# Optimization experiments

Hardware: AMD Instinct MI355X
Metric: run time of the kernel (lower is better)

The kernel has to match this reference:

```python
import jax, jax.numpy as jnp
import numpy as np

N_NODES = 50000
N_EDGES = 800000
N_GRAPHS = 256
IN_DIM = 128
HID = 128
BN_EPS = 1e-5


def setup_inputs() -> dict:
    key = jax.random.key(0)
    ks = jax.random.split(key, 12)
    s = 1.0 / np.sqrt(HID)
    feats = jax.random.normal(ks[0], (N_NODES, IN_DIM), jnp.float32)
    src = jax.random.randint(ks[1], (2, N_EDGES), 0, N_NODES)
    dst = jax.random.randint(ks[2], (2, N_EDGES), 0, N_NODES)
    graph_ids = jnp.sort(jax.random.randint(ks[3], (N_NODES,), 0, N_GRAPHS))
    eps = jnp.full((2, 2), 0.1, jnp.float32)
    Wa = jax.random.normal(ks[4], (2, 2, IN_DIM, HID), jnp.float32) * s
    ba = jnp.zeros((2, 2, HID), jnp.float32)
    bng = jnp.ones((2, 2, HID), jnp.float32)
    bnb = jnp.zeros((2, 2, HID), jnp.float32)
    Wb = jax.random.normal(ks[5], (2, 2, HID, HID), jnp.float32) * s
    bb = jnp.zeros((2, 2, HID), jnp.float32)
    oW1 = jax.random.normal(ks[6], (2 * HID, HID), jnp.float32) * (1.0 / np.sqrt(2 * HID))
    ob1 = jnp.zeros((HID,), jnp.float32)
    oW2 = jax.random.normal(ks[7], (HID, HID), jnp.float32) * s
    ob2 = jnp.zeros((HID,), jnp.float32)
    oW3 = jax.random.normal(ks[8], (HID, 1), jnp.float32) * s
    ob3 = jnp.zeros((1,), jnp.float32)
    return {"feats": feats, "src": src, "dst": dst, "graph_ids": graph_ids,
            "n_graphs": N_GRAPHS, "eps": eps, "Wa": Wa, "ba": ba, "bng": bng,
            "bnb": bnb, "Wb": Wb, "bb": bb, "oW1": oW1, "ob1": ob1,
            "oW2": oW2, "ob2": ob2, "oW3": oW3, "ob3": ob3}


def _gin_layer(h, s, d, eps_l, Wa_l, ba_l, g_l, be_l, Wb_l, bb_l, relu_out):
    # sum-aggregate messages from src to dst over edge list
    N = h.shape[0]
    agg = jax.ops.segment_sum(h[s], d, num_segments=N)  # [N, D]
    x = (1.0 + eps_l) * h + agg
    # MLP_Layer: Linear -> BatchNorm(training stats) -> ReLU -> Linear
    x = x @ Wa_l + ba_l
    mu = jnp.mean(x, axis=0)
    var = jnp.var(x, axis=0)
    x = (x - mu) * jax.lax.rsqrt(var + BN_EPS) * g_l + be_l
    x = jax.nn.relu(x)
    x = x @ Wb_l + bb_l
    return jax.nn.relu(x) if relu_out else x  # GINConv activation (gin1 only)


def reference(feats, src, dst, graph_ids, n_graphs, eps, Wa, ba, bng, bnb,
              Wb, bb, oW1, ob1, oW2, ob2, oW3, ob3):
    outs = []
    for e in range(2):  # one BTGINs encoder per bottom edge type
        h = feats
        for l in range(2):  # gin1 (ReLU) then gin2 (no activation)
            h = _gin_layer(h, src[e], dst[e], eps[e, l], Wa[e, l], ba[e, l],
                           bng[e, l], bnb[e, l], Wb[e, l], bb[e, l], relu_out=(l == 0))
        outs.append(h)
    h = jnp.concatenate(outs, axis=-1)  # [N, 2*HID]
    # readout_nodes op='sum': per-graph segment sum
    hg = jax.ops.segment_sum(h, graph_ids, num_segments=n_graphs)  # [G, 2*HID]
    # out_layers: 3-layer MLP, no BN
    x = jax.nn.relu(hg @ oW1 + ob1)
    x = jax.nn.relu(x @ oW2 + ob2)
    return x @ oW3 + ob3  # [G, 1]
```

## Files before the change

kernel.cpp:

```cpp
#include <hip/hip_runtime.h>

#define NT 50000
#define NE 800000
#define NG 256
#define DIM 128
#define GEMM_B ((NT + 127) / 128)

#define NB 128
#define BW 391
#define PB 196
#define PCH 4096
#define HCN (NB * PB)

typedef short s16x8 __attribute__((ext_vector_type(8)));
typedef float f32x16 __attribute__((ext_vector_type(16)));

__device__ __forceinline__ unsigned short f32_to_bf16(float f) {
    unsigned int u = __float_as_uint(f);
    u += 0x7FFFu + ((u >> 16) & 1u);
    return (unsigned short)(u >> 16);
}
__device__ __forceinline__ float bf16_to_f32(unsigned short h) {
    return __uint_as_float(((unsigned int)h) << 16);
}

__global__ __launch_bounds__(256) void tobf16_kernel(const float* __restrict__ in,
                                                     unsigned short* __restrict__ out) {
    int i = blockIdx.x * 256 + threadIdx.x;
    if (i >= NT * 32) return;
    float4 v = ((const float4*)in)[i];
    ushort4 o;
    o.x = f32_to_bf16(v.x); o.y = f32_to_bf16(v.y);
    o.z = f32_to_bf16(v.z); o.w = f32_to_bf16(v.w);
    ((ushort4*)out)[i] = o;
}

__global__ __launch_bounds__(256) void csr_part_hist_kernel(
        const int* __restrict__ dstAll, int* __restrict__ hcoarseAll) {
    const int* dst = dstAll + (size_t)blockIdx.y * NE;
    int* hcoarse = hcoarseAll + (size_t)blockIdx.y * HCN;
    __shared__ int h[NB];
    if (threadIdx.x < NB) h[threadIdx.x] = 0;
    __syncthreads();
#pragma unroll
    for (int i = 0; i < PCH / 256; ++i) {
        int e = blockIdx.x * PCH + i * 256 + threadIdx.x;
        if (e < NE) atomicAdd(&h[dst[e] / BW], 1);
    }
    __syncthreads();
    if (threadIdx.x < NB)
        hcoarse[threadIdx.x * PB + blockIdx.x] = h[threadIdx.x];
}

__global__ __launch_bounds__(1024) void csr_scan_kernel(
        const int* __restrict__ hcoarseAll, int* __restrict__ offAll,
        int* __restrict__ bucketBaseAll, int* __restrict__ indptrAll) {
    const int* hcoarse = hcoarseAll + (size_t)blockIdx.x * HCN;
    int* off = offAll + (size_t)blockIdx.x * HCN;
    int* bucketBase = bucketBaseAll + (size_t)blockIdx.x * (NB + 1);
    int* indptr = indptrAll + (size_t)blockIdx.x * (NT + 1);
    __shared__ int ps[1024];
    int t = threadIdx.x;
    const int CH = (HCN + 1023) / 1024;
    int beg = t * CH, end = beg + CH; if (end > HCN) end = HCN;
    int s = 0;
    for (int i = beg; i < end; ++i) s += hcoarse[i];
    ps[t] = s;
    __syncthreads();
    for (int o = 1; o < 1024; o <<= 1) {
        int v = (t >= o) ? ps[t - o] : 0;
        __syncthreads();
        ps[t] += v;
        __syncthreads();
    }
    int run = (t == 0) ? 0 : ps[t - 1];
    for (int i = beg; i < end; ++i) {
        off[i] = run;
        if (i % PB == 0) bucketBase[i / PB] = run;
        run += hcoarse[i];
    }
    if (t == 1023) bucketBase[NB] = NE;
    if (t == 0) indptr[NT] = NE;
}

__global__ __launch_bounds__(256) void csr_scatter_kernel(
        const int* __restrict__ srcAll, const int* __restrict__ dstAll,
        const int* __restrict__ offAll, unsigned int* __restrict__ partAll) {
    const int* src = srcAll + (size_t)blockIdx.y * NE;
    const int* dst = dstAll + (size_t)blockIdx.y * NE;
    const int* off = offAll + (size_t)blockIdx.y * HCN;
    unsigned int* part = partAll + (size_t)blockIdx.y * NE;
    __shared__ int cur[NB];
    if (threadIdx.x < NB) cur[threadIdx.x] = off[threadIdx.x * PB + blockIdx.x];
    __syncthreads();
#pragma unroll
    for (int i = 0; i < PCH / 256; ++i) {
        int e = blockIdx.x * PCH + i * 256 + threadIdx.x;
        if (e < NE) {
            int d = dst[e];
            int b = d / BW;
            int pos = atomicAdd(&cur[b], 1);
            part[pos] = ((unsigned int)(d - b * BW) << 16) | (unsigned int)src[e];
        }
    }
}

__global__ __launch_bounds__(256) void csr_finalize_kernel(
        const unsigned int* __restrict__ partAll,
        const int* __restrict__ bucketBaseAll,
        int* __restrict__ indptrAll, int* __restrict__ esrcAll) {
    const unsigned int* part = partAll + (size_t)blockIdx.y * NE;
    const int* bucketBase = bucketBaseAll + (size_t)blockIdx.y * (NB + 1);
    int* indptr = indptrAll + (size_t)blockIdx.y * (NT + 1);
    int* esrc = esrcAll + (size_t)blockIdx.y * NE;
    __shared__ int cnt[512];
    __shared__ int excl[512];
    __shared__ int ps[256];
    __shared__ int cur[BW + 1];
    int b = blockIdx.x, t = threadIdx.x;
    int base = bucketBase[b];
    int n = bucketBase[b + 1] - base;
    cnt[t] = 0; cnt[t + 256] = 0;
    for (int j = t; j <= BW; j += 256) cur[j] = 0;
    __syncthreads();
    for (int i = t; i < n; i += 256) atomicAdd(&cnt[part[base + i] >> 16], 1);
    __syncthreads();
    int a0 = cnt[2 * t], a1 = cnt[2 * t + 1];
    ps[t] = a0 + a1;
    __syncthreads();
    for (int o = 1; o < 256; o <<= 1) {
        int v = (t >= o) ? ps[t - o] : 0;
        __syncthreads();
        ps[t] += v;
        __syncthreads();
    }
    int before = (t == 0) ? 0 : ps[t - 1];
    excl[2 * t] = before;
    excl[2 * t + 1] = before + a0;
    __syncthreads();
    int node0 = b * BW;
    for (int j = t; j < BW; j += 256) {
        int gn = node0 + j;
        if (gn < NT) indptr[gn] = base + excl[j];
    }
    for (int i = t; i < n; i += 256) {
        unsigned int pk = part[base + i];
        int dl = pk >> 16;
        int pos = atomicAdd(&cur[dl], 1);
        esrc[base + excl[dl] + pos] = (int)(pk & 0xFFFFu);
    }
}

__global__ __launch_bounds__(256) void agg_split_kernel(
        const float* __restrict__ h, long hStride,
        const unsigned short* __restrict__ hb, long hbStride,
        const int* __restrict__ indptr2, const int* __restrict__ esrc2,
        const float* __restrict__ eps_p, int l,
        unsigned short* __restrict__ xout2) {
    int e = blockIdx.y;
    const float* hs = h + (size_t)e * hStride;
    const unsigned short* hbs = hb + (size_t)e * hbStride;
    const int* indptr = indptr2 + (size_t)e * (NT + 1);
    const int* esrc = esrc2 + (size_t)e * NE;
    unsigned short* xo = xout2 + (size_t)e * NT * 256;
    int node = blockIdx.x * 4 + (threadIdx.x >> 6);
    if (node >= NT) return;
    int lane = threadIdx.x & 63;
    int half = lane >> 5, c = lane & 31;
    float s0 = 0.f, s1 = 0.f, s2 = 0.f, s3 = 0.f;
    if (half == 0) {
        float e1 = 1.0f + eps_p[e * 2 + l];
        float4 a = ((const float4*)hs)[(size_t)node * 32 + c];
        s0 = e1 * a.x; s1 = e1 * a.y; s2 = e1 * a.z; s3 = e1 * a.w;
    }
    int beg = indptr[node], end = indptr[node + 1];
    int deg = end - beg;
    int endFull = beg + (deg & ~15);
    int j = beg;
    for (; j < endFull; j += 16) {
        int b0 = j + half * 8;
        int idx[8];
#pragma unroll
        for (int k = 0; k < 8; ++k) idx[k] = esrc[b0 + k];
        ushort4 v[8];
#pragma unroll
        for (int k = 0; k < 8; ++k)
            v[k] = *(const ushort4*)(hbs + (size_t)idx[k] * 128 + c * 4);
#pragma unroll
        for (int k = 0; k < 8; ++k) {
            s0 += bf16_to_f32(v[k].x);
            s1 += bf16_to_f32(v[k].y);
            s2 += bf16_to_f32(v[k].z);
            s3 += bf16_to_f32(v[k].w);
        }
    }
    if (j < end) {
        int b0 = j + half * 8;
        int idx[8];
        float m[8];
#pragma unroll
        for (int k = 0; k < 8; ++k) {
            int jj = b0 + k;
            int ok = jj < end;
            idx[k] = esrc[ok ? jj : end - 1];
            m[k] = ok ? 1.f : 0.f;
        }
        ushort4 v[8];
#pragma unroll
        for (int k = 0; k < 8; ++k)
            v[k] = *(const ushort4*)(hbs + (size_t)idx[k] * 128 + c * 4);
#pragma unroll
        for (int k = 0; k < 8; ++k) {
            s0 = fmaf(bf16_to_f32(v[k].x), m[k], s0);
            s1 = fmaf(bf16_to_f32(v[k].y), m[k], s1);
            s2 = fmaf(bf16_to_f32(v[k].z), m[k], s2);
            s3 = fmaf(bf16_to_f32(v[k].w), m[k], s3);
        }
    }
    s0 += __shfl_xor(s0, 32);
    s1 += __shfl_xor(s1, 32);
    s2 += __shfl_xor(s2, 32);
    s3 += __shfl_xor(s3, 32);
    if (half == 0) {
        ushort4 hv, lv;
        hv.x = f32_to_bf16(s0); lv.x = f32_to_bf16(s0 - bf16_to_f32(hv.x));
        hv.y = f32_to_bf16(s1); lv.y = f32_to_bf16(s1 - bf16_to_f32(hv.y));
        hv.z = f32_to_bf16(s2); lv.z = f32_to_bf16(s2 - bf16_to_f32(hv.z));
        hv.w = f32_to_bf16(s3); lv.w = f32_to_bf16(s3 - bf16_to_f32(hv.w));
        *(ushort4*)(xo + (size_t)node * 256 + c * 4) = hv;
        *(ushort4*)(xo + (size_t)node * 256 + 128 + c * 4) = lv;
    }
}

__global__ __launch_bounds__(256) void bsplit_kernel(const float* __restrict__ Wa,
                                                     const float* __restrict__ Wb,
                                                     unsigned short* __restrict__ Bfrag,
                                                     const int* __restrict__ gid,
                                                     int* __restrict__ goff,
                                                     float* __restrict__ gsumAll) {
    if (blockIdx.x == 0) {
        int g = threadIdx.x;
        int lo = 0, hi = NT;
        while (lo < hi) {
            int mid = (lo + hi) >> 1;
            if (gid[mid] < g) lo = mid + 1; else hi = mid;
        }
        goff[g] = lo;
        if (g == 0) goff[NG] = NT;
    }
    if (blockIdx.x == 1) {
#pragma unroll
        for (int i = 0; i < 4; ++i) gsumAll[i * 256 + threadIdx.x] = 0.f;
    }
    int slot = blockIdx.x >> 3;
    int sub = blockIdx.x & 7;
    const float* W = (slot < 4) ? (Wa + (size_t)slot * DIM * DIM)
                                : (Wb + (size_t)(slot - 4) * DIM * DIM);
    unsigned short* out = Bfrag + (size_t)slot * 32768;
    for (int i = 0; i < 16; ++i) {
        int e = sub * 4096 + i * 256 + threadIdx.x;
        int kphys = e >> 7, n = e & 127;
        int k = kphys & 127;
        float wv = W[k * 128 + n];
        unsigned short hi = f32_to_bf16(wv);
        unsigned short val = (kphys < 128) ? hi : f32_to_bf16(wv - bf16_to_f32(hi));
        int nt = n >> 5, nin = n & 31;
        int kcp = kphys >> 4, kgp = (kphys >> 3) & 1, jj = kphys & 7;
        out[(size_t)(((nt * 16 + kcp) * 64) + kgp * 32 + nin) * 8 + jj] = val;
    }
}

template <int ASPLIT, int STATS, int RELU, int EMITB, int FUSERO>
__global__ __launch_bounds__(256) void fused_gemm_kernel(
        const void* __restrict__ Asrc, long aStride,
        const unsigned short* __restrict__ BfragBase, int bOff, int l,
        const float* __restrict__ biasBase,
        const float* __restrict__ gsumBase,
        const float* __restrict__ gammaBase, const float* __restrict__ betaBase,
        float* __restrict__ C, long cStride,
        unsigned short* __restrict__ CBout, long cbStride,
        float* __restrict__ gsumOutBase,
        const int* __restrict__ gidIn, float* __restrict__ hgpOut) {
    __shared__ char smem[65536 + 1024 + 512];
    unsigned short* sB = (unsigned short*)smem;
    float* sBNa = (float*)(smem + 65536);
    float* sBNb = sBNa + 128;
    int* sgid = (int*)(smem + 65536 + 1024);
    const int ety = blockIdx.y, wi = ety * 2 + l;
    const unsigned short* Bfrag = BfragBase + (size_t)(bOff + wi) * 32768;
    const float* bias = biasBase + (size_t)wi * DIM;
    const int tid = threadIdx.x;
    const int w = tid >> 6, lane = tid & 63;
    const int nin = lane & 31, kg = lane >> 5;
    const int row0 = blockIdx.x * 128;
    const int myrow = row0 + w * 32 + nin;
    const int rowc = myrow < NT ? myrow : NT - 1;

    {
        const uint4* Bg = (const uint4*)Bfrag;
        uint4* sB4 = (uint4*)smem;
#pragma unroll
        for (int i = 0; i < 16; ++i) sB4[tid + 256 * i] = Bg[tid + 256 * i];
    }

    s16x8 ahi[8], alo[8];
    if (ASPLIT) {
        const unsigned short* ar = (const unsigned short*)Asrc
                + (size_t)ety * aStride + (size_t)rowc * 256 + kg * 8;
#pragma unroll
        for (int kc = 0; kc < 8; ++kc) {
            ahi[kc] = *(const s16x8*)(ar + kc * 16);
            alo[kc] = *(const s16x8*)(ar + 128 + kc * 16);
        }
        __syncthreads();
    } else {
        const float* gsumIn = gsumBase + (size_t)wi * 256;
        if (tid < 128) {
            float mu = gsumIn[tid] * (1.0f / NT);
            float var = gsumIn[128 + tid] * (1.0f / NT) - mu * mu;
            float inv = rsqrtf(var + 1e-5f);
            float a = gammaBase[wi * DIM + tid] * inv;
            sBNa[tid] = a;
            sBNb[tid] = betaBase[wi * DIM + tid] - mu * a;
            if (FUSERO) {
                int rr = row0 + tid;
                sgid[tid] = gidIn[rr < NT ? rr : NT - 1];
            }
        }
        __syncthreads();
        const float* yr = (const float*)Asrc + (size_t)ety * aStride
                + (size_t)rowc * 128 + kg * 8;
#pragma unroll
        for (int kc = 0; kc < 8; ++kc) {
            int c0 = kc * 16 + kg * 8;
            float4 y0 = *(const float4*)(yr + kc * 16);
            float4 y1 = *(const float4*)(yr + kc * 16 + 4);
            float4 a0 = *(const float4*)(sBNa + c0);
            float4 a1 = *(const float4*)(sBNa + c0 + 4);
            float4 b0 = *(const float4*)(sBNb + c0);
            float4 b1 = *(const float4*)(sBNb + c0 + 4);
            float t[8];
            t[0] = fmaxf(0.f, fmaf(y0.x, a0.x, b0.x));
            t[1] = fmaxf(0.f, fmaf(y0.y, a0.y, b0.y));
            t[2] = fmaxf(0.f, fmaf(y0.z, a0.z, b0.z));
            t[3] = fmaxf(0.f, fmaf(y0.w, a0.w, b0.w));
            t[4] = fmaxf(0.f, fmaf(y1.x, a1.x, b1.x));
            t[5] = fmaxf(0.f, fmaf(y1.y, a1.y, b1.y));
            t[6] = fmaxf(0.f, fmaf(y1.z, a1.z, b1.z));
            t[7] = fmaxf(0.f, fmaf(y1.w, a1.w, b1.w));
            union { s16x8 v; unsigned short u[8]; } H, L;
#pragma unroll
            for (int q = 0; q < 8; ++q) {
                H.u[q] = f32_to_bf16(t[q]);
                L.u[q] = f32_to_bf16(t[q] - bf16_to_f32(H.u[q]));
            }
            ahi[kc] = H.v; alo[kc] = L.v;
        }
    }

    f32x16 acc[4];
#pragma unroll
    for (int nt = 0; nt < 4; ++nt)
#pragma unroll
        for (int r = 0; r < 16; ++r) acc[nt][r] = 0.f;

#pragma unroll
    for (int nt = 0; nt < 4; ++nt) {
        const unsigned short* bp = sB + (size_t)(nt * 16) * 512 + lane * 8;
#pragma unroll
        for (int kc = 0; kc < 8; ++kc) {
            s16x8 b = *(const s16x8*)(bp + kc * 512);
            acc[nt] = __builtin_amdgcn_mfma_f32_32x32x16_bf16(ahi[kc], b, acc[nt], 0, 0, 0);
            acc[nt] = __builtin_amdgcn_mfma_f32_32x32x16_bf16(alo[kc], b, acc[nt], 0, 0, 0);
        }
#pragma unroll
        for (int kc = 0; kc < 8; ++kc) {
            s16x8 b = *(const s16x8*)(bp + (8 + kc) * 512);
            acc[nt] = __builtin_amdgcn_mfma_f32_32x32x16_bf16(ahi[kc], b, acc[nt], 0, 0, 0);
        }
    }

    if (FUSERO) {
#pragma unroll
        for (int nt = 0; nt < 4; ++nt) {
            int col = nt * 32 + nin;
            float bv = bias[col];
            float run = 0.f;
            int curg = -1;
#pragma unroll
            for (int reg = 0; reg < 16; ++reg) {
                int lr = w * 32 + 4 * kg + (reg & 3) + 8 * (reg >> 2);
                int gr = row0 + lr;
                float v = acc[nt][reg] + bv;
                int g = sgid[lr];
                if (g != curg) {
                    if (curg >= 0)
                        atomicAdd(&hgpOut[(size_t)curg * 256 + ety * 128 + col], run);
                    curg = g;
                    run = 0.f;
                }
                run += (gr < NT) ? v : 0.f;
            }
            if (curg >= 0)
                atomicAdd(&hgpOut[(size_t)curg * 256 + ety * 128 + col], run);
        }
        return;
    }

    float* Ce = C + (size_t)ety * cStride;
    unsigned short* CBe = EMITB ? (CBout + (size_t)ety * cbStride) : nullptr;
    const int rbase = row0 + w * 32 + 4 * kg;
#pragma unroll
    for (int nt = 0; nt < 4; ++nt) {
        int col = nt * 32 + nin;
        float bv = bias[col];
#pragma unroll
        for (int reg = 0; reg < 16; ++reg) {
            int gr = rbase + (reg & 3) + 8 * (reg >> 2);
            float v = acc[nt][reg] + bv;
            if (RELU) v = fmaxf(v, 0.f);
            if (gr < NT) {
                Ce[(size_t)gr * 128 + col] = v;
                if (EMITB) CBe[(size_t)gr * 128 + col] = f32_to_bf16(v);
            }
            acc[nt][reg] = (gr < NT) ? v : 0.f;
        }
    }

    if (STATS) {
        float* gsum = gsumOutBase + (size_t)wi * 256;
        __syncthreads();
        float* ls = (float*)smem;
        ls[tid] = 0.f;
        __syncthreads();
#pragma unroll
        for (int nt = 0; nt < 4; ++nt) {
            int col = nt * 32 + nin;
            float s = 0.f, q = 0.f;
#pragma unroll
            for (int reg = 0; reg < 16; ++reg) { float v = acc[nt][reg]; s += v; q += v * v; }
            atomicAdd(&ls[col], s);
            atomicAdd(&ls[128 + col], q);
        }
        __syncthreads();
        if (tid < 128) {
            atomicAdd(&gsum[tid], ls[tid]);
            atomicAdd(&gsum[128 + tid], ls[128 + tid]);
        }
    }
}

__global__ __launch_bounds__(128) void mlp_kernel(const float* __restrict__ hgp,
                                                  const float* __restrict__ oW1,
                                                  const float* __restrict__ ob1,
                                                  const float* __restrict__ oW2,
                                                  const float* __restrict__ ob2,
                                                  const float* __restrict__ oW3,
                                                  const float* __restrict__ ob3,
                                                  float* __restrict__ out) {
    int g = blockIdx.x, t = threadIdx.x;
    __shared__ float sh[256];
    __shared__ float z[128];
    sh[t] = hgp[g * 256 + t];
    sh[t + 128] = hgp[g * 256 + 128 + t];
    __syncthreads();
    float acc = ob1[t];
    for (int k = 0; k < 256; ++k) acc = fmaf(sh[k], oW1[k * 128 + t], acc);
    float z1 = fmaxf(acc, 0.f);
    z[t] = z1;
    __syncthreads();
    acc = ob2[t];
    for (int k = 0; k < 128; ++k) acc = fmaf(z[k], oW2[k * 128 + t], acc);
    float z2 = fmaxf(acc, 0.f);
    float p = z2 * oW3[t];
    for (int off = 32; off > 0; off >>= 1) p += __shfl_down(p, off, 64);
    __shared__ float wsum[2];
    if ((t & 63) == 0) wsum[t >> 6] = p;
    __syncthreads();
    if (t == 0) out[g] = wsum[0] + wsum[1] + ob3[0];
}

extern "C" void kernel_launch(void* const* d_in, const int* in_sizes, int n_in,
                              void* d_out, int out_size, void* d_ws, size_t ws_size,
                              hipStream_t stream) {
    (void)in_sizes; (void)n_in; (void)out_size; (void)ws_size;
    const float* feats = (const float*)d_in[0];
    const int*   src   = (const int*)d_in[1];
    const int*   dst   = (const int*)d_in[2];
    const int*   gid   = (const int*)d_in[3];
    const float* epsp  = (const float*)d_in[5];
    const float* Wa    = (const float*)d_in[6];
    const float* ba    = (const float*)d_in[7];
    const float* bng   = (const float*)d_in[8];
    const float* bnb   = (const float*)d_in[9];
    const float* Wb    = (const float*)d_in[10];
    const float* bb    = (const float*)d_in[11];
    const float* oW1   = (const float*)d_in[12];
    const float* ob1   = (const float*)d_in[13];
    const float* oW2   = (const float*)d_in[14];
    const float* ob2   = (const float*)d_in[15];
    const float* oW3   = (const float*)d_in[16];
    const float* ob3   = (const float*)d_in[17];
    float* out = (float*)d_out;

    char* p = (char*)d_ws;
    auto carve = [&](size_t bytes) -> void* {
        void* r = (void*)p;
        p += (bytes + 255) & ~(size_t)255;
        return r;
    };
    unsigned short* Asplit2 = (unsigned short*)carve((size_t)2 * NT * 256 * 2);
    float* bufY2   = (float*)carve((size_t)2 * NT * DIM * 4);
    float* bufH2   = (float*)carve((size_t)2 * NT * DIM * 4);
    unsigned short* featsB = (unsigned short*)carve((size_t)NT * DIM * 2);
    unsigned short* hB2    = (unsigned short*)carve((size_t)2 * NT * DIM * 2);
    unsigned short* Bfrag  = (unsigned short*)carve((size_t)8 * 32768 * 2);
    int*   esrc2    = (int*)carve((size_t)2 * NE * 4);
    unsigned int* part2 = (unsigned int*)carve((size_t)2 * NE * 4);
    int*   hcoarse2 = (int*)carve((size_t)2 * HCN * 4);
    int*   offbuf2  = (int*)carve((size_t)2 * HCN * 4);
    int*   bb2      = (int*)carve((size_t)2 * (NB + 1) * 4);
    int*   indptr2  = (int*)carve((size_t)2 * (NT + 1) * 4);
    int*   goff     = (int*)carve((size_t)(NG + 1) * 4);
    float* gsumAll  = (float*)carve((size_t)4 * 256 * 4);
    float* hgp      = (float*)carve((size_t)NG * 256 * 4);

    const int CB = (NT * 32 + 255) / 256;

    bsplit_kernel<<<64, 256, 0, stream>>>(Wa, Wb, Bfrag, gid, goff, gsumAll);
    tobf16_kernel<<<CB, 256, 0, stream>>>(feats, featsB);
    hipMemsetAsync(hgp, 0, (size_t)NG * 256 * 4, stream);

    csr_part_hist_kernel<<<dim3(PB, 2), 256, 0, stream>>>(dst, hcoarse2);
    csr_scan_kernel<<<2, 1024, 0, stream>>>(hcoarse2, offbuf2, bb2, indptr2);
    csr_scatter_kernel<<<dim3(PB, 2), 256, 0, stream>>>(src, dst, offbuf2, part2);
    csr_finalize_kernel<<<dim3(NB, 2), 256, 0, stream>>>(part2, bb2, indptr2, esrc2);

    for (int l = 0; l < 2; ++l) {
        if (l == 0)
            agg_split_kernel<<<dim3((NT + 3) / 4, 2), 256, 0, stream>>>(
                feats, 0, featsB, 0, indptr2, esrc2, epsp, l, Asplit2);
        else
            agg_split_kernel<<<dim3((NT + 3) / 4, 2), 256, 0, stream>>>(
                bufH2, (long)NT * DIM, hB2, (long)NT * DIM,
                indptr2, esrc2, epsp, l, Asplit2);
        fused_gemm_kernel<1, 1, 0, 0, 0><<<dim3(GEMM_B, 2), 256, 0, stream>>>(
            Asplit2, (long)NT * 256, Bfrag, 0, l, ba,
            nullptr, nullptr, nullptr,
            bufY2, (long)NT * DIM, nullptr, 0, gsumAll,
            nullptr, nullptr);
        if (l == 0)
            fused_gemm_kernel<0, 0, 1, 1, 0><<<dim3(GEMM_B, 2), 256, 0, stream>>>(
                bufY2, (long)NT * DIM, Bfrag, 4, l, bb,
                gsumAll, bng, bnb,
                bufH2, (long)NT * DIM, hB2, (long)NT * DIM, nullptr,
                nullptr, nullptr);
        else
            fused_gemm_kernel<0, 0, 0, 0, 1><<<dim3(GEMM_B, 2), 256, 0, stream>>>(
                bufY2, (long)NT * DIM, Bfrag, 4, l, bb,
                gsumAll, bng, bnb,
                nullptr, 0, nullptr, 0, nullptr,
                gid, hgp);
    }
    mlp_kernel<<<NG, 128, 0, stream>>>(hgp, oW1, ob1, oW2, ob2, oW3, ob3, out);
}
```

Measured before the change: 514.0 us.

## Merge setup launches into one kernel and widen gather unroll to 16 edges

Three setup operations (weight split, feature bf16 conversion, hgp memset) are fused into a single setup_kernel launch to cut launch and memset overhead. The aggregation kernel now processes 32 edges per iteration with each half-wave loading 16 interleaved neighbours, which raises memory-level parallelism in the gather. The larger unroll increases register pressure and pads low-degree tails with more masked loads.

```diff
diff --git a/kernel.cpp b/kernel.cpp
--- a/kernel.cpp
+++ b/kernel.cpp
@@ -22,17 +22,6 @@
 }
 __device__ __forceinline__ float bf16_to_f32(unsigned short h) {
     return __uint_as_float(((unsigned int)h) << 16);
-}
-
-__global__ __launch_bounds__(256) void tobf16_kernel(const float* __restrict__ in,
-                                                     unsigned short* __restrict__ out) {
-    int i = blockIdx.x * 256 + threadIdx.x;
-    if (i >= NT * 32) return;
-    float4 v = ((const float4*)in)[i];
-    ushort4 o;
-    o.x = f32_to_bf16(v.x); o.y = f32_to_bf16(v.y);
-    o.z = f32_to_bf16(v.z); o.w = f32_to_bf16(v.w);
-    ((ushort4*)out)[i] = o;
 }
 
 __global__ __launch_bounds__(256) void csr_part_hist_kernel(
@@ -175,19 +164,18 @@
     }
     int beg = indptr[node], end = indptr[node + 1];
     int deg = end - beg;
-    int endFull = beg + (deg & ~15);
+    int endFull = beg + (deg & ~31);
     int j = beg;
-    for (; j < endFull; j += 16) {
-        int b0 = j + half * 8;
-        int idx[8];
-#pragma unroll
-        for (int k = 0; k < 8; ++k) idx[k] = esrc[b0 + k];
-        ushort4 v[8];
-#pragma unroll
-        for (int k = 0; k < 8; ++k)
+    for (; j < endFull; j += 32) {
+        int idx[16];
+#pragma unroll
+        for (int k = 0; k < 16; ++k) idx[k] = esrc[j + 2 * k + half];
+        ushort4 v[16];
+#pragma unroll
+        for (int k = 0; k < 16; ++k)
             v[k] = *(const ushort4*)(hbs + (size_t)idx[k] * 128 + c * 4);
 #pragma unroll
-        for (int k = 0; k < 8; ++k) {
+        for (int k = 0; k < 16; ++k) {
             s0 += bf16_to_f32(v[k].x);
             s1 += bf16_to_f32(v[k].y);
             s2 += bf16_to_f32(v[k].z);
@@ -195,22 +183,21 @@
         }
     }
     if (j < end) {
-        int b0 = j + half * 8;
-        int idx[8];
-        float m[8];
-#pragma unroll
-        for (int k = 0; k < 8; ++k) {
-            int jj = b0 + k;
+        int idx[16];
+        float m[16];
+#pragma unroll
+        for (int k = 0; k < 16; ++k) {
+            int jj = j + 2 * k + half;
             int ok = jj < end;
             idx[k] = esrc[ok ? jj : end - 1];
             m[k] = ok ? 1.f : 0.f;
         }
-        ushort4 v[8];
-#pragma unroll
-        for (int k = 0; k < 8; ++k)
+        ushort4 v[16];
+#pragma unroll
+        for (int k = 0; k < 16; ++k)
             v[k] = *(const ushort4*)(hbs + (size_t)idx[k] * 128 + c * 4);
 #pragma unroll
-        for (int k = 0; k < 8; ++k) {
+        for (int k = 0; k < 16; ++k) {
             s0 = fmaf(bf16_to_f32(v[k].x), m[k], s0);
             s1 = fmaf(bf16_to_f32(v[k].y), m[k], s1);
             s2 = fmaf(bf16_to_f32(v[k].z), m[k], s2);
@@ -232,12 +219,26 @@
     }
 }
 
-__global__ __launch_bounds__(256) void bsplit_kernel(const float* __restrict__ Wa,
-                                                     const float* __restrict__ Wb,
-                                                     unsigned short* __restrict__ Bfrag,
-                                                     const int* __restrict__ gid,
-                                                     int* __restrict__ goff,
-                                                     float* __restrict__ gsumAll) {
+__global__ __launch_bounds__(256) void setup_kernel(const float* __restrict__ Wa,
+                                                    const float* __restrict__ Wb,
+                                                    unsigned short* __restrict__ Bfrag,
+                                                    const int* __restrict__ gid,
+                                                    int* __restrict__ goff,
+                                                    float* __restrict__ gsumAll,
+                                                    float* __restrict__ hgp,
+                                                    const float* __restrict__ feats,
+                                                    unsigned short* __restrict__ featsB) {
+    if (blockIdx.x >= 64) {
+        int i = (blockIdx.x - 64) * 256 + threadIdx.x;
+        if (i < NT * 32) {
+            float4 v = ((const float4*)feats)[i];
+            ushort4 o;
+            o.x = f32_to_bf16(v.x); o.y = f32_to_bf16(v.y);
+            o.z = f32_to_bf16(v.z); o.w = f32_to_bf16(v.w);
+            ((ushort4*)featsB)[i] = o;
+        }
+        return;
+    }
     if (blockIdx.x == 0) {
         int g = threadIdx.x;
         int lo = 0, hi = NT;
@@ -251,6 +252,17 @@
     if (blockIdx.x == 1) {
 #pragma unroll
         for (int i = 0; i < 4; ++i) gsumAll[i * 256 + threadIdx.x] = 0.f;
+    }
+    if (blockIdx.x >= 2 && blockIdx.x < 34) {
+        int base = (blockIdx.x - 2) * 2048 + threadIdx.x;
+        hgp[base] = 0.f;
+        hgp[base + 256] = 0.f;
+        hgp[base + 512] = 0.f;
+        hgp[base + 768] = 0.f;
+        hgp[base + 1024] = 0.f;
+        hgp[base + 1280] = 0.f;
+        hgp[base + 1536] = 0.f;
+        hgp[base + 1792] = 0.f;
     }
     int slot = blockIdx.x >> 3;
     int sub = blockIdx.x & 7;
@@ -527,9 +539,8 @@
 
     const int CB = (NT * 32 + 255) / 256;
 
-    bsplit_kernel<<<64, 256, 0, stream>>>(Wa, Wb, Bfrag, gid, goff, gsumAll);
-    tobf16_kernel<<<CB, 256, 0, stream>>>(feats, featsB);
-    hipMemsetAsync(hgp, 0, (size_t)NG * 256 * 4, stream);
+    setup_kernel<<<64 + CB, 256, 0, stream>>>(Wa, Wb, Bfrag, gid, goff,
+                                              gsumAll, hgp, feats, featsB);
 
     csr_part_hist_kernel<<<dim3(PB, 2), 256, 0, stream>>>(dst, hcoarse2);
     csr_scan_kernel<<<2, 1024, 0, stream>>>(hcoarse2, offbuf2, bb2, indptr2);
```

New measurement: 511.3 us. No clear change (-0.5%).
